# Kernel tuning notes

Measured on AMD Instinct MI355X. Metric: run time of the kernel, lower is better.

Reference implementation:

```python
import jax, jax.numpy as jnp
import numpy as np
from jax import lax

T = 16          # timesteps
EPS = 1e-12     # torch F.normalize eps
DN = ('NCHW', 'OIHW', 'NCHW')

def conv2d(x, w, pad):
    return lax.conv_general_dilated(x, w, (1, 1), [(pad, pad), (pad, pad)],
                                    dimension_numbers=DN)

def setup_inputs() -> dict:
    key = jax.random.key(0)
    ks = jax.random.split(key, 7)
    B, C, H, W, K = 16, 512, 14, 14, 64
    return {
        'input_tensor': jax.random.normal(ks[0], (B * T, C, H, W), jnp.float32),
        'centers': jax.random.normal(ks[1], (K, C), jnp.float32) * 0.05,
        'share_w': jax.random.normal(ks[2], (K, C, 1, 1), jnp.float32) * 0.05,
        'share_b': jax.random.uniform(ks[3], (K,), jnp.float32),
        'U_z': jax.random.normal(ks[4], (K, K, 3, 3), jnp.float32) * 0.05,
        'U_r': jax.random.normal(ks[5], (K, K, 3, 3), jnp.float32) * 0.05,
        'U_h': jax.random.normal(ks[6], (K, K, 3, 3), jnp.float32) * 0.05,
    }

def reference(input_tensor, centers, share_w, share_b, U_z, U_r, U_h):
    NT, C, H, W = input_tensor.shape
    B = NT // T
    K = centers.shape[0]

    # soft-assignment pre-activation: 1x1 conv (SAME) -> [B*T, K, H, W]
    wxb = conv2d(input_tensor, share_w, 0) + share_b[None, :, None, None]
    wxb = wxb.reshape(B, T, K, H, W).transpose(1, 0, 2, 3, 4)  # [T,B,K,H,W]

    def gru_step(h, wxb_t):
        z = jax.nn.sigmoid(wxb_t + conv2d(h, U_z, 1))
        r = jax.nn.sigmoid(wxb_t + conv2d(h, U_r, 1))
        hh = jnp.tanh(wxb_t + conv2d(r * h, U_h, 1))
        h_new = (1.0 - z) * hh + z * h
        return h_new, h_new

    h0 = jnp.zeros((B, K, H, W), input_tensor.dtype)
    _, assign = lax.scan(gru_step, h0, wxb)            # [T,B,K,H,W]
    assign = assign.transpose(1, 0, 2, 3, 4).reshape(B * T, K, H * W)

    a_sum = assign.sum(-1, keepdims=True)              # [BT,K,1]
    a = a_sum * centers[None]                          # [BT,K,C]
    feats = input_tensor.reshape(B * T, C, H * W)
    x = jnp.einsum('nks,ncs->nkc', assign, feats)      # [BT,K,C]

    vlad = (x - a).reshape(B, T, K, C).sum(1)          # [B,K,C]
    vlad = vlad / jnp.maximum(jnp.linalg.norm(vlad, axis=2, keepdims=True), EPS)
    vlad = vlad.reshape(B, K * C)
    vlad = vlad / jnp.maximum(jnp.linalg.norm(vlad, axis=1, keepdims=True), EPS)
    return vlad
```

## Files before the change

### kernel.cpp

```cpp
#include <hip/hip_runtime.h>

#define Bc 16
#define Tc 16
#define Cc 512
#define Kc 64
#define Sc 196
#define KS (Kc*Sc)
#define BKS (Bc*Kc*Sc)
#define TBKS (Tc*BKS)
#define GFIN (16*64*512)
#define PART_N (8*GFIN)
#define PX 256
#define PLB2 (Kc*PX)

__device__ __forceinline__ float sigmoid_f(float x) { return 1.f / (1.f + __expf(-x)); }
__device__ __forceinline__ float tanh_f(float x) { return 1.f - 2.f / (__expf(2.f * x) + 1.f); }

__device__ __forceinline__ float dpp_prev(float v) {
    return __int_as_float(__builtin_amdgcn_mov_dpp(__float_as_int(v), 0x111, 0xf, 0xf, true));
}
__device__ __forceinline__ float dpp_next(float v) {
    return __int_as_float(__builtin_amdgcn_mov_dpp(__float_as_int(v), 0x101, 0xf, 0xf, true));
}

__global__ __launch_bounds__(256) void k_transpose_w(const float* __restrict__ w, float* __restrict__ wt) {
    int idx = blockIdx.x * 256 + threadIdx.x;
    if (idx < Kc * Cc) {
        int k = idx & 63, c = idx >> 6;
        wt[idx] = w[k * Cc + c];
    }
}

__global__ __launch_bounds__(256) void k_conv1x1(const float* __restrict__ x, const float* __restrict__ wt,
                                                 const float* __restrict__ bias, float* __restrict__ wxb) {
    __shared__ float Xs[64][64];
    const int tid = threadIdx.x;
    const int gs0 = blockIdx.x * 64;
    const int kw = __builtin_amdgcn_readfirstlane((tid >> 6) << 4);
    const int lane = tid & 63;
    const int rbase = (tid >> 6) * 16;
    const int gs_c = gs0 + lane;
    const int n_c = gs_c / Sc, s_c = gs_c - n_c * Sc;
    const float* xcol = x + (size_t)n_c * (Cc * Sc) + s_c;

    float xr[16];
#pragma unroll
    for (int q = 0; q < 16; ++q) xr[q] = xcol[(size_t)(rbase + q) * Sc];
    float acc[16] = {};
    for (int c0 = 0; c0 < Cc; c0 += 64) {
        __syncthreads();
#pragma unroll
        for (int q = 0; q < 16; ++q) Xs[rbase + q][lane] = xr[q];
        __syncthreads();
        if (c0 + 64 < Cc) {
#pragma unroll
            for (int q = 0; q < 16; ++q) xr[q] = xcol[(size_t)(c0 + 64 + rbase + q) * Sc];
        }
#pragma unroll 8
        for (int cc = 0; cc < 64; ++cc) {
            const float xv = Xs[cc][lane];
            const float* wp = wt + (size_t)(c0 + cc) * Kc + kw;
#pragma unroll
            for (int i = 0; i < 16; ++i) acc[i] += wp[i] * xv;
        }
    }
    const int t = n_c & 15, bb = n_c >> 4;
    float* op = wxb + (((size_t)t * Bc + bb) * Kc + kw) * Sc + s_c;
#pragma unroll
    for (int i = 0; i < 16; ++i)
        op[(size_t)i * Sc] = acc[i] + bias[kw + i];
}

__global__ __launch_bounds__(64) void k_gru_t0(const float* __restrict__ wxb,
        float* __restrict__ hplane, float* __restrict__ rhplane, float* __restrict__ assign) {
    const int blk = blockIdx.x;
    const size_t pbase = (size_t)blk * PX;
    const size_t cbase = (size_t)blk * Sc;
    for (int i = threadIdx.x; i < PX; i += 64) {
        int row = i >> 4, col = i & 15;
        float v = 0.f;
        if (row >= 1 && row <= 14 && col >= 1 && col <= 14) {
            int s = (row - 1) * 14 + (col - 1);
            float pre = wxb[cbase + s];
            v = (1.f - sigmoid_f(pre)) * tanh_f(pre);
            assign[cbase + s] = v;
        }
        hplane[pbase + i] = v;
        rhplane[pbase + i] = 0.f;
    }
}

__global__ __launch_bounds__(512) void k_gru_gates(const float* __restrict__ hplane,
        const float* __restrict__ wxb_t, const float* __restrict__ Uz, const float* __restrict__ Ur,
        float* __restrict__ zb, float* __restrict__ rhplane) {
    extern __shared__ float lds[];
    float* P = lds;
    float* red = lds + PLB2;
    const int b = blockIdx.x;
    const int k = blockIdx.y;
    const int tid = threadIdx.x;
    const int wv = __builtin_amdgcn_readfirstlane(tid >> 6);
    const int lane = tid & 63;

    const int setE = tid >> 8;
    const int pxE = tid & 255;
    const int rE = pxE >> 4, xbE = pxE & 15;
    const bool valE = (rE >= 1 && rE <= 14 && xbE >= 1 && xbE <= 14);
    const size_t cbase = ((size_t)b * Kc + k) * Sc;
    const int sE = (rE - 1) * 14 + (xbE - 1);
    const float preE = valE ? wxb_t[cbase + sE] : 0.f;

    {
        const float4* src = (const float4*)(hplane + (size_t)b * PLB2);
        float4* dst = (float4*)P;
#pragma unroll
        for (int it = 0; it < 8; ++it) dst[it * 512 + tid] = src[it * 512 + tid];
    }
    __syncthreads();

    const int yp = lane >> 2, xq = (lane & 3) << 2;
    const int rowbase = (yp > 0) ? (yp - 1) : 0;
    const float* uzb = Uz + (size_t)k * 576 + wv * 72;
    const float* urb = Ur + (size_t)k * 576 + wv * 72;
    float az[4] = {}, ar[4] = {};
    const float* Pw = P + (size_t)(wv * 8) * PX + rowbase * 16 + xq;
#pragma unroll 2
    for (int ki8 = 0; ki8 < 8; ++ki8) {
        const float* pk = Pw + ki8 * PX;
#pragma unroll
        for (int dy = 0; dy < 3; ++dy) {
            float4 m = *(const float4*)(pk + dy * 16);
            float e0 = dpp_prev(m.w);
            float e4 = dpp_next(m.x);
            const float* wz = uzb + ki8 * 9 + dy * 3;
            float c0 = wz[0], c1 = wz[1], c2 = wz[2];
            az[0] += c0*e0  + c1*m.x + c2*m.y;
            az[1] += c0*m.x + c1*m.y + c2*m.z;
            az[2] += c0*m.y + c1*m.z + c2*m.w;
            az[3] += c0*m.z + c1*m.w + c2*e4;
            const float* wr = urb + ki8 * 9 + dy * 3;
            float d0 = wr[0], d1 = wr[1], d2 = wr[2];
            ar[0] += d0*e0  + d1*m.x + d2*m.y;
            ar[1] += d0*m.x + d1*m.y + d2*m.z;
            ar[2] += d0*m.y + d1*m.z + d2*m.w;
            ar[3] += d0*m.z + d1*m.w + d2*e4;
        }
    }
    {
        float* rp = red + (size_t)wv * 512 + lane * 4;
        *(float4*)rp = make_float4(az[0], az[1], az[2], az[3]);
        *(float4*)(rp + 256) = make_float4(ar[0], ar[1], ar[2], ar[3]);
    }
    __syncthreads();
    {
        const float* q = red + setE * 256 + pxE;
        float s0 = 0.f;
#pragma unroll
        for (int w8 = 0; w8 < 8; ++w8) s0 += q[(size_t)w8 * 512];
        if (valE) {
            float sv = sigmoid_f(preE + s0);
            if (setE == 0) {
                zb[cbase + sE] = sv;
            } else {
                float hv = P[(size_t)k * PX + pxE];
                rhplane[(size_t)b * PLB2 + (size_t)k * PX + pxE] = sv * hv;
            }
        }
    }
}

__global__ __launch_bounds__(512) void k_gru_out(const float* __restrict__ rhplane,
        const float* __restrict__ wxb_t, const float* __restrict__ Uh, const float* __restrict__ zb,
        float* __restrict__ hplane, float* __restrict__ assign_t) {
    extern __shared__ float lds[];
    float* P = lds;
    float* red = lds + PLB2;
    const int b = blockIdx.x;
    const int k = blockIdx.y;
    const int tid = threadIdx.x;
    const int wv = __builtin_amdgcn_readfirstlane(tid >> 6);
    const int lane = tid & 63;

    const bool epi = (tid < 256);
    const int pxE = tid & 255;
    const int rE = pxE >> 4, xbE = pxE & 15;
    const bool valE = epi && (rE >= 1 && rE <= 14 && xbE >= 1 && xbE <= 14);
    const size_t cbase = ((size_t)b * Kc + k) * Sc;
    const size_t pbase = (size_t)b * PLB2 + (size_t)k * PX;
    const int sE = (rE - 1) * 14 + (xbE - 1);
    float preE = 0.f, zvE = 0.f, hpE = 0.f;
    if (valE) {
        preE = wxb_t[cbase + sE];
        zvE = zb[cbase + sE];
        hpE = hplane[pbase + pxE];
    }
    {
        const float4* src = (const float4*)(rhplane + (size_t)b * PLB2);
        float4* dst = (float4*)P;
#pragma unroll
        for (int it = 0; it < 8; ++it) dst[it * 512 + tid] = src[it * 512 + tid];
    }
    __syncthreads();

    const int yp = lane >> 2, xq = (lane & 3) << 2;
    const int rowbase = (yp > 0) ? (yp - 1) : 0;
    const float* uhb = Uh + (size_t)k * 576 + wv * 72;
    float ah[4] = {};
    const float* Pw = P + (size_t)(wv * 8) * PX + rowbase * 16 + xq;
#pragma unroll 2
    for (int ki8 = 0; ki8 < 8; ++ki8) {
        const float* pk = Pw + ki8 * PX;
#pragma unroll
        for (int dy = 0; dy < 3; ++dy) {
            float4 m = *(const float4*)(pk + dy * 16);
            float e0 = dpp_prev(m.w);
            float e4 = dpp_next(m.x);
            const float* wh = uhb + ki8 * 9 + dy * 3;
            float c0 = wh[0], c1 = wh[1], c2 = wh[2];
            ah[0] += c0*e0  + c1*m.x + c2*m.y;
            ah[1] += c0*m.x + c1*m.y + c2*m.z;
            ah[2] += c0*m.y + c1*m.z + c2*m.w;
            ah[3] += c0*m.z + c1*m.w + c2*e4;
        }
    }
    {
        float* rp = red + (size_t)wv * 256 + lane * 4;
        *(float4*)rp = make_float4(ah[0], ah[1], ah[2], ah[3]);
    }
    __syncthreads();
    if (epi) {
        const float* q = red + pxE;
        float s0 = 0.f;
#pragma unroll
        for (int w8 = 0; w8 < 8; ++w8) s0 += q[(size_t)w8 * 256];
        if (valE) {
            float hh = tanh_f(preE + s0);
            float hn = (1.f - zvE) * hh + zvE * hpE;
            hplane[pbase + pxE] = hn;
            assign_t[cbase + sE] = hn;
        }
    }
}

__global__ __launch_bounds__(256) void k_einsum(const float* __restrict__ x, const float* __restrict__ assign,
                                                float* __restrict__ part) {
    extern __shared__ float lds[];
    float* As = lds;
    float* Xs = lds + 196 * 68;
    const int ch = blockIdx.x, tg = blockIdx.y, b = blockIdx.z;
    const int tid = threadIdx.x;
    const int w = tid >> 6, lane = tid & 63;
    const int kt3 = lane >> 3, ct3 = lane & 7;
    const int kbase = kt3 * 8;
    const int cbase = w * 32 + ct3 * 4;
    float4 acc[8] = {};
    for (int tt = 0; tt < 2; ++tt) {
        const int t = tg * 2 + tt;
        const int n = b * Tc + t;
        __syncthreads();
        {
            const float* ap = assign + ((size_t)t * Bc + b) * KS;
            for (int q = tid; q < 3136; q += 256) {
                int kq = q / Sc, s = q - kq * Sc;
                int k4 = kq * 4;
                float4 v;
                v.x = ap[(size_t)(k4 + 0) * Sc + s];
                v.y = ap[(size_t)(k4 + 1) * Sc + s];
                v.z = ap[(size_t)(k4 + 2) * Sc + s];
                v.w = ap[(size_t)(k4 + 3) * Sc + s];
                *(float4*)(As + (size_t)s * 68 + k4) = v;
            }
        }
        for (int sc = 0; sc < 7; ++sc) {
            const int sb = sc * 28;
            __syncthreads();
            {
                const int c = tid & 127, sh = tid >> 7;
                const float* xp = x + ((size_t)n * Cc + ch * 128 + c) * Sc + sb + sh * 16;
                const int nf = sh ? 3 : 4;
                for (int f = 0; f < nf; ++f) {
                    float4 v = *(const float4*)(xp + f * 4);
                    float* dst = Xs + (size_t)(sh * 16 + f * 4) * 132 + c;
                    dst[0] = v.x; dst[132] = v.y; dst[264] = v.z; dst[396] = v.w;
                }
            }
            __syncthreads();
#pragma unroll 4
            for (int s = 0; s < 28; ++s) {
                const float* ap = As + (size_t)(sb + s) * 68 + kbase;
                float4 a0 = *(const float4*)ap;
                float4 a1 = *(const float4*)(ap + 4);
                float4 xv = *(const float4*)(Xs + (size_t)s * 132 + cbase);
                float av[8] = {a0.x,a0.y,a0.z,a0.w,a1.x,a1.y,a1.z,a1.w};
#pragma unroll
                for (int i = 0; i < 8; ++i) {
                    acc[i].x += av[i] * xv.x;
                    acc[i].y += av[i] * xv.y;
                    acc[i].z += av[i] * xv.z;
                    acc[i].w += av[i] * xv.w;
                }
            }
        }
    }
#pragma unroll
    for (int i = 0; i < 8; ++i) {
        const int k = kbase + i;
        float* op = part + (((size_t)tg * Bc + b) * Kc + k) * Cc + ch * 128 + cbase;
        *(float4*)op = acc[i];
    }
}

__global__ __launch_bounds__(256) void k_reduce(const float* __restrict__ assign, const float* __restrict__ part,
        const float* __restrict__ centers, float* __restrict__ vlad, float* __restrict__ norm2) {
    __shared__ float redw[4];
    __shared__ float a_s;
    const int blk = blockIdx.x;
    const int b = blk >> 6, k = blk & 63;
    const int tid = threadIdx.x;
    const int wave = tid >> 6, lane = tid & 63;
    const size_t bkoff = ((size_t)b * Kc + k) * Sc;
    float s = 0.f;
    for (int q = tid; q < 784; q += 256) {
        int t = q / 49, s4 = q - t * 49;
        float4 v = *(const float4*)(assign + (size_t)t * BKS + bkoff + s4 * 4);
        s += (v.x + v.y) + (v.z + v.w);
    }
#pragma unroll
    for (int o = 1; o < 64; o <<= 1) s += __shfl_xor(s, o);
    if (lane == 0) redw[wave] = s;
    __syncthreads();
    if (tid == 0) a_s = redw[0] + redw[1] + redw[2] + redw[3];
    __syncthreads();
    const float a = a_s;
    const size_t base = ((size_t)b * Kc + k) * Cc;
    const int c = tid * 2;
    float2 acc2 = make_float2(0.f, 0.f);
#pragma unroll
    for (int g = 0; g < 8; ++g) {
        float2 p = *(const float2*)(part + (size_t)g * GFIN + base + c);
        acc2.x += p.x; acc2.y += p.y;
    }
    float2 cv = *(const float2*)(centers + (size_t)k * Cc + c);
    float v0 = acc2.x - a * cv.x, v1 = acc2.y - a * cv.y;
    *(float2*)(vlad + base + c) = make_float2(v0, v1);
    float ss = v0 * v0 + v1 * v1;
#pragma unroll
    for (int o = 1; o < 64; o <<= 1) ss += __shfl_xor(ss, o);
    __syncthreads();
    if (lane == 0) redw[wave] = ss;
    __syncthreads();
    if (tid == 0) norm2[blk] = redw[0] + redw[1] + redw[2] + redw[3];
}

__global__ __launch_bounds__(64) void k_norms(const float* __restrict__ norm2, float* __restrict__ scl) {
    const int b = blockIdx.x;
    const int k = threadIdx.x;
    float ss = norm2[b * Kc + k];
    float inv = 1.f / fmaxf(sqrtf(ss), 1e-12f);
    float g = ss * inv * inv;
#pragma unroll
    for (int o = 1; o < 64; o <<= 1) g += __shfl_xor(g, o);
    float gi = 1.f / fmaxf(sqrtf(g), 1e-12f);
    scl[b * Kc + k] = inv * gi;
}

__global__ __launch_bounds__(256) void k_scale(const float* __restrict__ vlad, const float* __restrict__ scl,
                                               float* __restrict__ out) {
    const int blk = blockIdx.x;
    const int b = blk >> 4, kt = blk & 15;
    const int tid = threadIdx.x;
    const int kk = tid >> 6, lane = tid & 63;
    const int k = kt * 4 + kk;
    const float sv = scl[b * Kc + k];
    const float* vp = vlad + ((size_t)b * Kc + k) * Cc + lane * 8;
    float* op = out + ((size_t)b * Kc + k) * Cc + lane * 8;
    float4 v0 = *(const float4*)vp;
    float4 v1 = *(const float4*)(vp + 4);
    *(float4*)op = make_float4(v0.x * sv, v0.y * sv, v0.z * sv, v0.w * sv);
    *(float4*)(op + 4) = make_float4(v1.x * sv, v1.y * sv, v1.z * sv, v1.w * sv);
}

extern "C" void kernel_launch(void* const* d_in, const int* in_sizes, int n_in,
                              void* d_out, int out_size, void* d_ws, size_t ws_size,
                              hipStream_t stream) {
    (void)in_sizes; (void)n_in; (void)out_size; (void)ws_size;
    const float* x       = (const float*)d_in[0];
    const float* centers = (const float*)d_in[1];
    const float* share_w = (const float*)d_in[2];
    const float* share_b = (const float*)d_in[3];
    const float* Uz      = (const float*)d_in[4];
    const float* Ur      = (const float*)d_in[5];
    const float* Uh      = (const float*)d_in[6];
    float* out = (float*)d_out;
    float* ws  = (float*)d_ws;

    float* part    = ws;
    float* vlad    = ws;
    float* wxb     = ws;
    float* rhplane = ws + (size_t)TBKS;
    float* assign  = ws + (size_t)PART_N;
    float* zb      = assign + (size_t)TBKS;
    float* hplane  = zb + (size_t)BKS;
    float* wt      = hplane + (size_t)Bc * PLB2;
    float* norm2   = wt + (size_t)Kc * Cc;
    float* scl     = norm2 + (size_t)Bc * Kc;

    const size_t gates_lds = (size_t)(PLB2 + 8 * 2 * 256) * 4;
    const size_t outk_lds  = (size_t)(PLB2 + 8 * 256) * 4;
    const size_t ein_lds   = (size_t)(196 * 68 + 28 * 132) * 4;

    k_transpose_w<<<dim3(128), 256, 0, stream>>>(share_w, wt);
    k_conv1x1<<<dim3(784), 256, 0, stream>>>(x, wt, share_b, wxb);
    k_gru_t0<<<dim3(1024), 64, 0, stream>>>(wxb, hplane, rhplane, assign);
    for (int t = 1; t < Tc; ++t) {
        k_gru_gates<<<dim3(16, 64), 512, gates_lds, stream>>>(hplane, wxb + (size_t)t * BKS,
                                                              Uz, Ur, zb, rhplane);
        k_gru_out<<<dim3(16, 64), 512, outk_lds, stream>>>(rhplane, wxb + (size_t)t * BKS,
                                                           Uh, zb, hplane, assign + (size_t)t * BKS);
    }
    k_einsum<<<dim3(4, 8, 16), 256, ein_lds, stream>>>(x, assign, part);
    k_reduce<<<dim3(Bc * Kc), 256, 0, stream>>>(assign, part, centers, vlad, norm2);
    k_norms<<<dim3(Bc), 64, 0, stream>>>(norm2, scl);
    k_scale<<<dim3(256), 256, 0, stream>>>(vlad, scl, out);
}
```

Before: 464.6 us.

## Store GRU hidden planes in bf16 and compute four output channels per block

The recurrent conv kernels now stage the hidden state and the r*h state in LDS as bf16 and convert to fp32 when reading. This halves the global and LDS traffic per block. Each block now computes 4 output channels instead of 1, with each wave handling 2 channels over 16 input channels, so the staged plane is reused across more outputs and the grid shrinks from 1024 to 256 blocks. An fp32 copy of h is kept for the blend step, but the conv inputs lose precision to bf16, which may push results past tolerance.

After: 459.3 us. About the same (-1.1%).

```diff
diff --git a/kernel.cpp b/kernel.cpp
--- a/kernel.cpp
+++ b/kernel.cpp
@@ -16,6 +16,14 @@
 __device__ __forceinline__ float sigmoid_f(float x) { return 1.f / (1.f + __expf(-x)); }
 __device__ __forceinline__ float tanh_f(float x) { return 1.f - 2.f / (__expf(2.f * x) + 1.f); }
 
+__device__ __forceinline__ float b2f(unsigned short u) {
+    return __uint_as_float(((unsigned)u) << 16);
+}
+__device__ __forceinline__ unsigned short f2b(float f) {
+    unsigned u = __float_as_uint(f);
+    return (unsigned short)((u + 0x7FFFu + ((u >> 16) & 1u)) >> 16);
+}
+
 __device__ __forceinline__ float dpp_prev(float v) {
     return __int_as_float(__builtin_amdgcn_mov_dpp(__float_as_int(v), 0x111, 0xf, 0xf, true));
 }
@@ -72,7 +80,8 @@
 }
 
 __global__ __launch_bounds__(64) void k_gru_t0(const float* __restrict__ wxb,
-        float* __restrict__ hplane, float* __restrict__ rhplane, float* __restrict__ assign) {
+        float* __restrict__ hplane32, unsigned short* __restrict__ hplane16,
+        unsigned short* __restrict__ rhplane16, float* __restrict__ assign) {
     const int blk = blockIdx.x;
     const size_t pbase = (size_t)blk * PX;
     const size_t cbase = (size_t)blk * Sc;
@@ -85,159 +94,202 @@
             v = (1.f - sigmoid_f(pre)) * tanh_f(pre);
             assign[cbase + s] = v;
         }
-        hplane[pbase + i] = v;
-        rhplane[pbase + i] = 0.f;
-    }
-}
-
-__global__ __launch_bounds__(512) void k_gru_gates(const float* __restrict__ hplane,
+        hplane32[pbase + i] = v;
+        hplane16[pbase + i] = f2b(v);
+        rhplane16[pbase + i] = 0;
+    }
+}
+
+__global__ __launch_bounds__(512) void k_gru_gates(const unsigned short* __restrict__ hplane16,
         const float* __restrict__ wxb_t, const float* __restrict__ Uz, const float* __restrict__ Ur,
-        float* __restrict__ zb, float* __restrict__ rhplane) {
+        float* __restrict__ zb, unsigned short* __restrict__ rhplane16) {
     extern __shared__ float lds[];
-    float* P = lds;
-    float* red = lds + PLB2;
+    unsigned short* P = (unsigned short*)lds;
+    float* red = lds + 8192;
     const int b = blockIdx.x;
-    const int k = blockIdx.y;
+    const int k0 = blockIdx.y * 4;
     const int tid = threadIdx.x;
     const int wv = __builtin_amdgcn_readfirstlane(tid >> 6);
     const int lane = tid & 63;
-
-    const int setE = tid >> 8;
-    const int pxE = tid & 255;
-    const int rE = pxE >> 4, xbE = pxE & 15;
-    const bool valE = (rE >= 1 && rE <= 14 && xbE >= 1 && xbE <= 14);
-    const size_t cbase = ((size_t)b * Kc + k) * Sc;
-    const int sE = (rE - 1) * 14 + (xbE - 1);
-    const float preE = valE ? wxb_t[cbase + sE] : 0.f;
-
+    const int kp = wv >> 2, kiq = wv & 3;
+
+    float preE[4]; bool valE[4]; size_t csE[4]; int kEa[4];
+#pragma unroll
+    for (int q = 0; q < 4; ++q) {
+        const int o = tid + q * 512;
+        const int set = o >> 8, px = o & 255;
+        const int kp_o = set >> 2, r = set & 1;
+        kEa[q] = k0 + kp_o * 2 + r;
+        const int row = px >> 4, col = px & 15;
+        valE[q] = (row >= 1 && row <= 14 && col >= 1 && col <= 14);
+        csE[q] = ((size_t)b * Kc + kEa[q]) * Sc + (valE[q] ? (row - 1) * 14 + (col - 1) : 0);
+        preE[q] = valE[q] ? wxb_t[csE[q]] : 0.f;
+    }
     {
-        const float4* src = (const float4*)(hplane + (size_t)b * PLB2);
+        const float4* src = (const float4*)(hplane16 + (size_t)b * PLB2);
         float4* dst = (float4*)P;
 #pragma unroll
-        for (int it = 0; it < 8; ++it) dst[it * 512 + tid] = src[it * 512 + tid];
+        for (int it = 0; it < 4; ++it) dst[it * 512 + tid] = src[it * 512 + tid];
     }
     __syncthreads();
 
     const int yp = lane >> 2, xq = (lane & 3) << 2;
     const int rowbase = (yp > 0) ? (yp - 1) : 0;
-    const float* uzb = Uz + (size_t)k * 576 + wv * 72;
-    const float* urb = Ur + (size_t)k * 576 + wv * 72;
-    float az[4] = {}, ar[4] = {};
-    const float* Pw = P + (size_t)(wv * 8) * PX + rowbase * 16 + xq;
+    const float* uz0 = Uz + (size_t)(k0 + kp * 2) * 576 + kiq * 144;
+    const float* ur0 = Ur + (size_t)(k0 + kp * 2) * 576 + kiq * 144;
+    float az[2][4] = {}, ar[2][4] = {};
+    const unsigned short* Pw = P + (size_t)(kiq * 16) * PX + rowbase * 16 + xq;
 #pragma unroll 2
-    for (int ki8 = 0; ki8 < 8; ++ki8) {
-        const float* pk = Pw + ki8 * PX;
+    for (int ki = 0; ki < 16; ++ki) {
+        const unsigned short* pk = Pw + ki * PX;
 #pragma unroll
         for (int dy = 0; dy < 3; ++dy) {
-            float4 m = *(const float4*)(pk + dy * 16);
+            ushort4 u = *(const ushort4*)(pk + dy * 16);
+            float4 m = make_float4(b2f(u.x), b2f(u.y), b2f(u.z), b2f(u.w));
             float e0 = dpp_prev(m.w);
             float e4 = dpp_next(m.x);
-            const float* wz = uzb + ki8 * 9 + dy * 3;
-            float c0 = wz[0], c1 = wz[1], c2 = wz[2];
-            az[0] += c0*e0  + c1*m.x + c2*m.y;
-            az[1] += c0*m.x + c1*m.y + c2*m.z;
-            az[2] += c0*m.y + c1*m.z + c2*m.w;
-            az[3] += c0*m.z + c1*m.w + c2*e4;
-            const float* wr = urb + ki8 * 9 + dy * 3;
-            float d0 = wr[0], d1 = wr[1], d2 = wr[2];
-            ar[0] += d0*e0  + d1*m.x + d2*m.y;
-            ar[1] += d0*m.x + d1*m.y + d2*m.z;
-            ar[2] += d0*m.y + d1*m.z + d2*m.w;
-            ar[3] += d0*m.z + d1*m.w + d2*e4;
+#pragma unroll
+            for (int r = 0; r < 2; ++r) {
+                const float* wz = uz0 + r * 576 + ki * 9 + dy * 3;
+                float c0 = wz[0], c1 = wz[1], c2 = wz[2];
+                az[r][0] += c0*e0  + c1*m.x + c2*m.y;
+                az[r][1] += c0*m.x + c1*m.y + c2*m.z;
+                az[r][2] += c0*m.y + c1*m.z + c2*m.w;
+                az[r][3] += c0*m.z + c1*m.w + c2*e4;
+                const float* wr = ur0 + r * 576 + ki * 9 + dy * 3;
+                float d0 = wr[0], d1 = wr[1], d2 = wr[2];
+                ar[r][0] += d0*e0  + d1*m.x + d2*m.y;
+                ar[r][1] += d0*m.x + d1*m.y + d2*m.z;
+                ar[r][2] += d0*m.y + d1*m.z + d2*m.w;
+                ar[r][3] += d0*m.z + d1*m.w + d2*e4;
+            }
         }
     }
     {
-        float* rp = red + (size_t)wv * 512 + lane * 4;
-        *(float4*)rp = make_float4(az[0], az[1], az[2], az[3]);
-        *(float4*)(rp + 256) = make_float4(ar[0], ar[1], ar[2], ar[3]);
-    }
-    __syncthreads();
-    {
-        const float* q = red + setE * 256 + pxE;
+        float* rp = red + (size_t)wv * 1024 + lane;
+#pragma unroll
+        for (int r = 0; r < 2; ++r)
+#pragma unroll
+            for (int jj = 0; jj < 4; ++jj) {
+                rp[(size_t)(r * 4 + jj) * 64] = az[r][jj];
+                rp[(size_t)(8 + r * 4 + jj) * 64] = ar[r][jj];
+            }
+    }
+    __syncthreads();
+#pragma unroll
+    for (int q = 0; q < 4; ++q) {
+        const int o = tid + q * 512;
+        const int set = o >> 8, px = o & 255;
+        const int kp_o = set >> 2, g = (set >> 1) & 1, r = set & 1;
+        const int lane_r = ((px >> 4) << 2) + ((px & 15) >> 2);
+        const int v = (g * 2 + r) * 4 + (px & 3);
         float s0 = 0.f;
 #pragma unroll
-        for (int w8 = 0; w8 < 8; ++w8) s0 += q[(size_t)w8 * 512];
-        if (valE) {
-            float sv = sigmoid_f(preE + s0);
-            if (setE == 0) {
-                zb[cbase + sE] = sv;
+        for (int kq2 = 0; kq2 < 4; ++kq2)
+            s0 += red[(size_t)((kp_o * 4 + kq2) * 16 + v) * 64 + lane_r];
+        if (valE[q]) {
+            float sv = sigmoid_f(preE[q] + s0);
+            if (g == 0) {
+                zb[csE[q]] = sv;
             } else {
-                float hv = P[(size_t)k * PX + pxE];
-                rhplane[(size_t)b * PLB2 + (size_t)k * PX + pxE] = sv * hv;
-            }
-        }
-    }
-}
-
-__global__ __launch_bounds__(512) void k_gru_out(const float* __restrict__ rhplane,
+                float hv = b2f(P[(size_t)kEa[q] * PX + px]);
+                rhplane16[(size_t)b * PLB2 + (size_t)kEa[q] * PX + px] = f2b(sv * hv);
+            }
+        }
+    }
+}
+
+__global__ __launch_bounds__(512) void k_gru_out(const unsigned short* __restrict__ rhplane16,
         const float* __restrict__ wxb_t, const float* __restrict__ Uh, const float* __restrict__ zb,
-        float* __restrict__ hplane, float* __restrict__ assign_t) {
+        float* __restrict__ hplane32, unsigned short* __restrict__ hplane16,
+        float* __restrict__ assign_t) {
     extern __shared__ float lds[];
-    float* P = lds;
-    float* red = lds + PLB2;
+    unsigned short* P = (unsigned short*)lds;
+    float* red = lds + 8192;
     const int b = blockIdx.x;
-    const int k = blockIdx.y;
+    const int k0 = blockIdx.y * 4;
     const int tid = threadIdx.x;
     const int wv = __builtin_amdgcn_readfirstlane(tid >> 6);
     const int lane = tid & 63;
-
-    const bool epi = (tid < 256);
-    const int pxE = tid & 255;
-    const int rE = pxE >> 4, xbE = pxE & 15;
-    const bool valE = epi && (rE >= 1 && rE <= 14 && xbE >= 1 && xbE <= 14);
-    const size_t cbase = ((size_t)b * Kc + k) * Sc;
-    const size_t pbase = (size_t)b * PLB2 + (size_t)k * PX;
-    const int sE = (rE - 1) * 14 + (xbE - 1);
-    float preE = 0.f, zvE = 0.f, hpE = 0.f;
-    if (valE) {
-        preE = wxb_t[cbase + sE];
-        zvE = zb[cbase + sE];
-        hpE = hplane[pbase + pxE];
+    const int kp = wv >> 2, kiq = wv & 3;
+
+    float preE[2], zvE[2], hpE[2]; bool valE[2]; size_t csE[2], ppE[2];
+#pragma unroll
+    for (int q = 0; q < 2; ++q) {
+        const int o = tid + q * 512;
+        const int set = o >> 8, px = o & 255;
+        const int kp_o = set >> 1, r = set & 1;
+        const int k = k0 + kp_o * 2 + r;
+        const int row = px >> 4, col = px & 15;
+        valE[q] = (row >= 1 && row <= 14 && col >= 1 && col <= 14);
+        csE[q] = ((size_t)b * Kc + k) * Sc + (valE[q] ? (row - 1) * 14 + (col - 1) : 0);
+        ppE[q] = (size_t)b * PLB2 + (size_t)k * PX + px;
+        preE[q] = 0.f; zvE[q] = 0.f; hpE[q] = 0.f;
+        if (valE[q]) {
+            preE[q] = wxb_t[csE[q]];
+            zvE[q] = zb[csE[q]];
+            hpE[q] = hplane32[ppE[q]];
+        }
     }
     {
-        const float4* src = (const float4*)(rhplane + (size_t)b * PLB2);
+        const float4* src = (const float4*)(rhplane16 + (size_t)b * PLB2);
         float4* dst = (float4*)P;
 #pragma unroll
-        for (int it = 0; it < 8; ++it) dst[it * 512 + tid] = src[it * 512 + tid];
+        for (int it = 0; it < 4; ++it) dst[it * 512 + tid] = src[it * 512 + tid];
     }
     __syncthreads();
 
     const int yp = lane >> 2, xq = (lane & 3) << 2;
     const int rowbase = (yp > 0) ? (yp - 1) : 0;
-    const float* uhb = Uh + (size_t)k * 576 + wv * 72;
-    float ah[4] = {};
-    const float* Pw = P + (size_t)(wv * 8) * PX + rowbase * 16 + xq;
+    const float* uh0 = Uh + (size_t)(k0 + kp * 2) * 576 + kiq * 144;
+    float ah[2][4] = {};
+    const unsigned short* Pw = P + (size_t)(kiq * 16) * PX + rowbase * 16 + xq;
 #pragma unroll 2
-    for (int ki8 = 0; ki8 < 8; ++ki8) {
-        const float* pk = Pw + ki8 * PX;
+    for (int ki = 0; ki < 16; ++ki) {
+        const unsigned short* pk = Pw + ki * PX;
 #pragma unroll
         for (int dy = 0; dy < 3; ++dy) {
-            float4 m = *(const float4*)(pk + dy * 16);
+            ushort4 u = *(const ushort4*)(pk + dy * 16);
+            float4 m = make_float4(b2f(u.x), b2f(u.y), b2f(u.z), b2f(u.w));
             float e0 = dpp_prev(m.w);
             float e4 = dpp_next(m.x);
-            const float* wh = uhb + ki8 * 9 + dy * 3;
-            float c0 = wh[0], c1 = wh[1], c2 = wh[2];
-            ah[0] += c0*e0  + c1*m.x + c2*m.y;
-            ah[1] += c0*m.x + c1*m.y + c2*m.z;
-            ah[2] += c0*m.y + c1*m.z + c2*m.w;
-            ah[3] += c0*m.z + c1*m.w + c2*e4;
+#pragma unroll
+            for (int r = 0; r < 2; ++r) {
+                const float* wh = uh0 + r * 576 + ki * 9 + dy * 3;
+                float c0 = wh[0], c1 = wh[1], c2 = wh[2];
+                ah[r][0] += c0*e0  + c1*m.x + c2*m.y;
+                ah[r][1] += c0*m.x + c1*m.y + c2*m.z;
+                ah[r][2] += c0*m.y + c1*m.z + c2*m.w;
+                ah[r][3] += c0*m.z + c1*m.w + c2*e4;
+            }
         }
     }
     {
-        float* rp = red + (size_t)wv * 256 + lane * 4;
-        *(float4*)rp = make_float4(ah[0], ah[1], ah[2], ah[3]);
-    }
-    __syncthreads();
-    if (epi) {
-        const float* q = red + pxE;
+        float* rp = red + (size_t)wv * 512 + lane;
+#pragma unroll
+        for (int r = 0; r < 2; ++r)
+#pragma unroll
+            for (int jj = 0; jj < 4; ++jj)
+                rp[(size_t)(r * 4 + jj) * 64] = ah[r][jj];
+    }
+    __syncthreads();
+#pragma unroll
+    for (int q = 0; q < 2; ++q) {
+        const int o = tid + q * 512;
+        const int set = o >> 8, px = o & 255;
+        const int kp_o = set >> 1, r = set & 1;
+        const int lane_r = ((px >> 4) << 2) + ((px & 15) >> 2);
+        const int v = r * 4 + (px & 3);
         float s0 = 0.f;
 #pragma unroll
-        for (int w8 = 0; w8 < 8; ++w8) s0 += q[(size_t)w8 * 256];
-        if (valE) {
-            float hh = tanh_f(preE + s0);
-            float hn = (1.f - zvE) * hh + zvE * hpE;
-            hplane[pbase + pxE] = hn;
-            assign_t[cbase + sE] = hn;
+        for (int kq2 = 0; kq2 < 4; ++kq2)
+            s0 += red[(size_t)((kp_o * 4 + kq2) * 8 + v) * 64 + lane_r];
+        if (valE[q]) {
+            float hh = tanh_f(preE[q] + s0);
+            float hn = (1.f - zvE[q]) * hh + zvE[q] * hpE[q];
+            hplane32[ppE[q]] = hn;
+            hplane16[ppE[q]] = f2b(hn);
+            assign_t[csE[q]] = hn;
         }
     }
 }
@@ -394,29 +446,31 @@
     float* out = (float*)d_out;
     float* ws  = (float*)d_ws;
 
-    float* part    = ws;
-    float* vlad    = ws;
-    float* wxb     = ws;
-    float* rhplane = ws + (size_t)TBKS;
-    float* assign  = ws + (size_t)PART_N;
-    float* zb      = assign + (size_t)TBKS;
-    float* hplane  = zb + (size_t)BKS;
-    float* wt      = hplane + (size_t)Bc * PLB2;
-    float* norm2   = wt + (size_t)Kc * Cc;
-    float* scl     = norm2 + (size_t)Bc * Kc;
-
-    const size_t gates_lds = (size_t)(PLB2 + 8 * 2 * 256) * 4;
-    const size_t outk_lds  = (size_t)(PLB2 + 8 * 256) * 4;
+    float* part      = ws;
+    float* vlad      = ws;
+    float* wxb       = ws;
+    unsigned short* rhplane16 = (unsigned short*)(ws + (size_t)TBKS);
+    unsigned short* hplane16  = (unsigned short*)(ws + (size_t)TBKS + 131072);
+    float* assign   = ws + (size_t)PART_N;
+    float* zb       = assign + (size_t)TBKS;
+    float* hplane32 = zb + (size_t)BKS;
+    float* wt       = hplane32 + (size_t)Bc * PLB2;
+    float* norm2    = wt + (size_t)Kc * Cc;
+    float* scl      = norm2 + (size_t)Bc * Kc;
+
+    const size_t gates_lds = 65536;
+    const size_t outk_lds  = 49152;
     const size_t ein_lds   = (size_t)(196 * 68 + 28 * 132) * 4;
 
     k_transpose_w<<<dim3(128), 256, 0, stream>>>(share_w, wt);
     k_conv1x1<<<dim3(784), 256, 0, stream>>>(x, wt, share_b, wxb);
-    k_gru_t0<<<dim3(1024), 64, 0, stream>>>(wxb, hplane, rhplane, assign);
+    k_gru_t0<<<dim3(1024), 64, 0, stream>>>(wxb, hplane32, hplane16, rhplane16, assign);
     for (int t = 1; t < Tc; ++t) {
-        k_gru_gates<<<dim3(16, 64), 512, gates_lds, stream>>>(hplane, wxb + (size_t)t * BKS,
-                                                              Uz, Ur, zb, rhplane);
-        k_gru_out<<<dim3(16, 64), 512, outk_lds, stream>>>(rhplane, wxb + (size_t)t * BKS,
-                                                           Uh, zb, hplane, assign + (size_t)t * BKS);
+        k_gru_gates<<<dim3(16, 16), 512, gates_lds, stream>>>(hplane16, wxb + (size_t)t * BKS,
+                                                              Uz, Ur, zb, rhplane16);
+        k_gru_out<<<dim3(16, 16), 512, outk_lds, stream>>>(rhplane16, wxb + (size_t)t * BKS,
+                                                           Uh, zb, hplane32, hplane16,
+                                                           assign + (size_t)t * BKS);
     }
     k_einsum<<<dim3(4, 8, 16), 256, ein_lds, stream>>>(x, assign, part);
     k_reduce<<<dim3(Bc * Kc), 256, 0, stream>>>(assign, part, centers, vlad, norm2);
```
